# Kernel optimization log

Hardware: AMD Instinct MI355X
Metric: run time of the kernel (lower is better)

Reference implementation:

```python
import jax, jax.numpy as jnp
import numpy as np

EPS = 1e-06

def _feature_map(x):
    # elu(x) + 1, positive feature map
    return jax.nn.elu(x) + 1.0

def setup_inputs() -> dict:
    key = jax.random.key(0)
    k1, k2, k3 = jax.random.split(key, 3)
    B, L, d_k, d_v = 2, 4096, 128, 128
    Q = jax.random.normal(k1, (B, L, d_k), dtype=jnp.float32)
    K = jax.random.normal(k2, (B, L, d_k), dtype=jnp.float32)
    V = jax.random.normal(k3, (B, L, d_v), dtype=jnp.float32)
    return {"Q": Q, "K": K, "V": V}

def reference(Q, K, V):
    # Causal linear attention (ELU feature map).
    # out_l = phi(Q_l) @ sum_{j<=l} phi(K_j)^T V_j
    # Z_l   = phi(Q_l) . sum_{j<=l} phi(K_j)
    phiQ = _feature_map(Q)                       # (B, L, dk)
    phiK = _feature_map(K)                       # (B, L, dk)
    # cumulative KV state: (B, L, dk, dv) -- parallel replacement of the
    # original per-step bmm loop
    KV = jnp.cumsum(phiK[..., :, None] * V[..., None, :], axis=1)
    out = jnp.einsum('blk,blkv->blv', phiQ, KV)  # (B, L, dv)
    Kc = jnp.cumsum(phiK, axis=1)                # (B, L, dk)
    Z = jnp.einsum('blk,blk->bl', phiQ, Kc)[..., None]  # (B, L, 1)
    return out / (Z + EPS)
```

## Files before the change

### kernel.cpp

```cpp
#include <hip/hip_runtime.h>


#define EPS 1e-6f

constexpr int Bc = 2;
constexpr int L  = 4096;
constexpr int D  = 128;
constexpr int C  = 128;
constexpr int NC = L / C;
constexpr int P  = 136;

typedef short sh8 __attribute__((ext_vector_type(8)));
typedef float f4  __attribute__((ext_vector_type(4)));

__device__ __forceinline__ float phi(float x) {
    return x > 0.0f ? x + 1.0f : __expf(x);
}
__device__ __forceinline__ unsigned short f2bf(float f) {
    unsigned u = __float_as_uint(f);
    return (unsigned short)((u + 0x7FFFu + ((u >> 16) & 1u)) >> 16);
}
__device__ __forceinline__ float bf2f(unsigned short h) {
    return __uint_as_float(((unsigned)h) << 16);
}
__device__ __forceinline__ unsigned packbf(float a, float b) {
    return (unsigned)f2bf(a) | ((unsigned)f2bf(b) << 16);
}
__device__ __forceinline__ sh8 splat1() {
    sh8 s;
#pragma unroll
    for (int j = 0; j < 8; ++j) s[j] = (short)0x3F80;
    return s;
}

__global__ __launch_bounds__(512) void k1(
    const float* __restrict__ K, const float* __restrict__ V,
    unsigned short* __restrict__ SB, float* __restrict__ Ksum) {
    const int c = blockIdx.x, b = blockIdx.y, vs = blockIdx.z;
    const int tid = threadIdx.x;
    __shared__ __align__(16) unsigned short sVT[64 * P];
    __shared__ __align__(16) unsigned short sKT[128 * P];
    const size_t base = ((size_t)b * L + (size_t)c * C) * D;

    for (int k = 0; k < 4; ++k) {
        int fi = tid + 512 * k;
        int l = fi >> 4, c4 = fi & 15;
        float4 vd = *(const float4*)(V + base + (size_t)l * D + vs * 64 + c4 * 4);
        int blk = (((l >> 3) + c4) & 15) * 8 + (l & 7);
        sVT[(c4 * 4 + 0) * P + blk] = f2bf(vd.x);
        sVT[(c4 * 4 + 1) * P + blk] = f2bf(vd.y);
        sVT[(c4 * 4 + 2) * P + blk] = f2bf(vd.z);
        sVT[(c4 * 4 + 3) * P + blk] = f2bf(vd.w);
    }
    for (int k = 0; k < 8; ++k) {
        int fi = tid + 512 * k;
        int l = fi >> 5, i4 = fi & 31;
        float4 kd = *(const float4*)(K + base + (size_t)l * D + i4 * 4);
        int blk = (((l >> 3) + i4) & 15) * 8 + (l & 7);
        sKT[(i4 * 4 + 0) * P + blk] = f2bf(phi(kd.x));
        sKT[(i4 * 4 + 1) * P + blk] = f2bf(phi(kd.y));
        sKT[(i4 * 4 + 2) * P + blk] = f2bf(phi(kd.z));
        sKT[(i4 * 4 + 3) * P + blk] = f2bf(phi(kd.w));
    }
    __syncthreads();

    const int w = tid >> 6, lane = tid & 63;
    const int r = lane & 15, q = lane >> 4;
    const int rbase = (w & 3) * 16;
    const int cbase = (w >> 2) * 64;
    const bool doK = ((w & 3) == 0);
    const sh8 ones = splat1();

    f4 acc[4], kz[4];
#pragma unroll
    for (int f = 0; f < 4; ++f) { acc[f] = {0.f,0.f,0.f,0.f}; kz[f] = {0.f,0.f,0.f,0.f}; }
#pragma unroll
    for (int ks = 0; ks < 4; ++ks) {
        int kq = ks * 4 + q;
        int vr = rbase + r;
        sh8 a = *(const sh8*)(sVT + vr * P + ((kq + (vr >> 2)) & 15) * 8);
#pragma unroll
        for (int f = 0; f < 4; ++f) {
            int ir = cbase + f * 16 + r;
            sh8 bk = *(const sh8*)(sKT + ir * P + ((kq + (ir >> 2)) & 15) * 8);
            acc[f] = __builtin_amdgcn_mfma_f32_16x16x32_bf16(a, bk, acc[f], 0, 0, 0);
            if (doK) kz[f] = __builtin_amdgcn_mfma_f32_16x16x32_bf16(ones, bk, kz[f], 0, 0, 0);
        }
    }
    unsigned short* out = SB + ((size_t)(b * NC + c)) * D * D;
#pragma unroll
    for (int f = 0; f < 4; ++f) {
        int i = cbase + f * 16 + r;
#pragma unroll
        for (int e = 0; e < 4; ++e) {
            int v = vs * 64 + rbase + q * 4 + e;
            out[(size_t)v * D + i] = f2bf(acc[f][e]);
        }
    }
    if (doK && q == 0 && vs == 0) {
#pragma unroll
        for (int f = 0; f < 4; ++f)
            Ksum[((size_t)(b * NC + c)) * D + cbase + f * 16 + r] = kz[f][0];
    }
}

__global__ __launch_bounds__(256) void k_scan(unsigned short* __restrict__ SB,
                                              float* __restrict__ Ksum) {
    const int SD = D * D;
    int idx = blockIdx.x * 256 + threadIdx.x;
    if (idx < Bc * SD) {
        int b = idx / SD, e = idx % SD;
        size_t off0 = (size_t)b * NC * SD + e;
        unsigned short vals[NC];
#pragma unroll
        for (int c = 0; c < NC; ++c) vals[c] = SB[off0 + (size_t)c * SD];
        float run = 0.0f;
#pragma unroll
        for (int c = 0; c < NC; ++c) {
            SB[off0 + (size_t)c * SD] = f2bf(run);
            run += bf2f(vals[c]);
        }
    } else if (idx < Bc * SD + Bc * D) {
        int rr = idx - Bc * SD;
        int b = rr >> 7, i = rr & 127;
        size_t off0 = (size_t)b * NC * D + i;
        float vals[NC];
#pragma unroll
        for (int c = 0; c < NC; ++c) vals[c] = Ksum[off0 + (size_t)c * D];
        float run = 0.0f;
#pragma unroll
        for (int c = 0; c < NC; ++c) {
            Ksum[off0 + (size_t)c * D] = run;
            run += vals[c];
        }
    }
}

__global__ __launch_bounds__(512) void k_out(
    const float* __restrict__ Q, const float* __restrict__ K,
    const float* __restrict__ V, const unsigned short* __restrict__ SB,
    const float* __restrict__ Ksum, float* __restrict__ Out) {
    const int c = blockIdx.x, b = blockIdx.y, rs = blockIdx.z;
    const int tid = threadIdx.x;
    __shared__ __align__(16) unsigned short sQ[32 * P];
    __shared__ __align__(16) unsigned short sK[128 * P];
    __shared__ __align__(16) unsigned short sVT[128 * P];
    __shared__ __align__(16) unsigned short sAm[32 * P];
    __shared__ float sZ[32];
    const size_t base  = ((size_t)b * L + (size_t)c * C) * D;
    const size_t tbase = ((size_t)(b * NC + c)) * (size_t)D * D;
    const size_t kb    = ((size_t)(b * NC + c)) * D;

    for (int k = 0; k < 2; ++k) {
        int fi = tid + 512 * k;
        int row = fi >> 5, c4 = fi & 31;
        float4 qd = *(const float4*)(Q + base + (size_t)(rs * 32 + row) * D + c4 * 4);
        uint2 pq; pq.x = packbf(phi(qd.x), phi(qd.y)); pq.y = packbf(phi(qd.z), phi(qd.w));
        *(uint2*)(sQ + row * P + c4 * 4) = pq;
    }
    for (int k = 0; k < 8; ++k) {
        int fi = tid + 512 * k;
        int row = fi >> 5, c4 = fi & 31;
        float4 kd = *(const float4*)(K + base + (size_t)row * D + c4 * 4);
        uint2 pk; pk.x = packbf(phi(kd.x), phi(kd.y)); pk.y = packbf(phi(kd.z), phi(kd.w));
        *(uint2*)(sK + row * P + c4 * 4) = pk;
    }
    for (int k = 0; k < 8; ++k) {
        int fi = tid + 512 * k;
        int l = fi >> 5, i4 = fi & 31;
        float4 vd = *(const float4*)(V + base + (size_t)l * D + i4 * 4);
        int blk = (((l >> 3) + i4) & 15) * 8 + (l & 7);
        sVT[(i4 * 4 + 0) * P + blk] = f2bf(vd.x);
        sVT[(i4 * 4 + 1) * P + blk] = f2bf(vd.y);
        sVT[(i4 * 4 + 2) * P + blk] = f2bf(vd.z);
        sVT[(i4 * 4 + 3) * P + blk] = f2bf(vd.w);
    }
    __syncthreads();

    const int w = tid >> 6, lane = tid & 63;
    const int r = lane & 15, q = lane >> 4;
    const int rbase = (w & 1) * 16;
    const int cq = w >> 1, cbase = cq * 32;
    const bool doZ = (cq == 3);

    sh8 bzk[4];
    if (doZ) {
#pragma unroll
        for (int ks = 0; ks < 4; ++ks) {
            float4 f0 = *(const float4*)(Ksum + kb + ks * 32 + q * 8);
            float4 f1 = *(const float4*)(Ksum + kb + ks * 32 + q * 8 + 4);
            sh8 t;
            t[0] = (short)f2bf(f0.x); t[1] = (short)f2bf(f0.y);
            t[2] = (short)f2bf(f0.z); t[3] = (short)f2bf(f0.w);
            t[4] = (short)f2bf(f1.x); t[5] = (short)f2bf(f1.y);
            t[6] = (short)f2bf(f1.z); t[7] = (short)f2bf(f1.w);
            bzk[ks] = t;
        }
    }

    f4 a2[2];
#pragma unroll
    for (int f = 0; f < 2; ++f) a2[f] = {0.f,0.f,0.f,0.f};
#pragma unroll
    for (int ks = 0; ks < 4; ++ks) {
        sh8 a = *(const sh8*)(sQ + (rbase + r) * P + ks * 32 + q * 8);
#pragma unroll
        for (int f = 0; f < 2; ++f) {
            sh8 bb = *(const sh8*)(sK + (cbase + f * 16 + r) * P + ks * 32 + q * 8);
            a2[f] = __builtin_amdgcn_mfma_f32_16x16x32_bf16(a, bb, a2[f], 0, 0, 0);
        }
    }
#pragma unroll
    for (int f = 0; f < 2; ++f) {
        int j = cbase + f * 16 + r;
#pragma unroll
        for (int e = 0; e < 4; ++e) {
            int lr = rbase + q * 4 + e;
            sAm[lr * P + j] = f2bf((j <= rs * 32 + lr) ? a2[f][e] : 0.f);
        }
    }
    __syncthreads();

    {
        const uint4* sg = (const uint4*)(SB + tbase);
        for (int k = 0; k < 4; ++k) {
            int f2 = tid + 512 * k;
            *(uint4*)(sK + (f2 >> 4) * P + (f2 & 15) * 8) = sg[f2];
        }
    }

    f4 acc[2], zacc = {0.f,0.f,0.f,0.f};
#pragma unroll
    for (int f = 0; f < 2; ++f) acc[f] = {0.f,0.f,0.f,0.f};
    const sh8 ones = splat1();
#pragma unroll
    for (int ks = 0; ks < 4; ++ks) {
        int kq = ks * 4 + q;
        sh8 a = *(const sh8*)(sAm + (rbase + r) * P + ks * 32 + q * 8);
#pragma unroll
        for (int f = 0; f < 2; ++f) {
            int vr = cbase + f * 16 + r;
            sh8 bv = *(const sh8*)(sVT + vr * P + ((kq + (vr >> 2)) & 15) * 8);
            acc[f] = __builtin_amdgcn_mfma_f32_16x16x32_bf16(a, bv, acc[f], 0, 0, 0);
        }
        if (doZ) zacc = __builtin_amdgcn_mfma_f32_16x16x32_bf16(a, ones, zacc, 0, 0, 0);
    }
    __syncthreads();

#pragma unroll
    for (int ks = 0; ks < 4; ++ks) {
        sh8 a = *(const sh8*)(sQ + (rbase + r) * P + ks * 32 + q * 8);
#pragma unroll
        for (int f = 0; f < 2; ++f) {
            sh8 bs = *(const sh8*)(sK + (cbase + f * 16 + r) * P + ks * 32 + q * 8);
            acc[f] = __builtin_amdgcn_mfma_f32_16x16x32_bf16(a, bs, acc[f], 0, 0, 0);
        }
        if (doZ) zacc = __builtin_amdgcn_mfma_f32_16x16x32_bf16(a, bzk[ks], zacc, 0, 0, 0);
    }
    if (doZ && r == 0) {
#pragma unroll
        for (int e = 0; e < 4; ++e) sZ[rbase + q * 4 + e] = zacc[e] + EPS;
    }
    __syncthreads();

#pragma unroll
    for (int f = 0; f < 2; ++f) {
        int v = cbase + f * 16 + r;
#pragma unroll
        for (int e = 0; e < 4; ++e) {
            int lr = rbase + q * 4 + e;
            Out[base + (size_t)(rs * 32 + lr) * D + v] = acc[f][e] / sZ[lr];
        }
    }
}

extern "C" void kernel_launch(void* const* d_in, const int* in_sizes, int n_in,
                              void* d_out, int out_size, void* d_ws, size_t ws_size,
                              hipStream_t stream) {
    const float* Q = (const float*)d_in[0];
    const float* K = (const float*)d_in[1];
    const float* V = (const float*)d_in[2];
    float* Out = (float*)d_out;
    unsigned short* SBw = (unsigned short*)d_ws;
    float* Ksum = (float*)((char*)d_ws + (size_t)Bc * NC * D * D * 2);

    k1<<<dim3(NC, Bc, 2), 512, 0, stream>>>(K, V, SBw, Ksum);
    int total = Bc * D * D + Bc * D;
    k_scan<<<dim3((total + 255) / 256), 256, 0, stream>>>(SBw, Ksum);
    k_out<<<dim3(NC, Bc, 4), 512, 0, stream>>>(Q, K, V, SBw, Ksum, Out);
}
```

Before: 77.56 us.

## Precompute bf16 phi(K) and transposed V in k1, read directly from global in k_out

k1 now also writes bf16 phi(K) rows and the swizzled bf16 V-transpose tile to workspace. k_out drops its shared-memory staging of Q, K, V and the scan state and reads MFMA operands straight from global/L2, keeping phi(Q) fragments in registers. This removes the redundant fp32 loads and conversions of K and V that the four row-split blocks each repeated, along with several barriers. The cost is extra global writes in k1, more workspace, and uncoalesced 16-byte operand loads from L2 inside the MFMA loops.

```diff
diff --git a/kernel.cpp b/kernel.cpp
--- a/kernel.cpp
+++ b/kernel.cpp
@@ -23,9 +23,6 @@
 __device__ __forceinline__ float bf2f(unsigned short h) {
     return __uint_as_float(((unsigned)h) << 16);
 }
-__device__ __forceinline__ unsigned packbf(float a, float b) {
-    return (unsigned)f2bf(a) | ((unsigned)f2bf(b) << 16);
-}
 __device__ __forceinline__ sh8 splat1() {
     sh8 s;
 #pragma unroll
@@ -35,7 +32,8 @@
 
 __global__ __launch_bounds__(512) void k1(
     const float* __restrict__ K, const float* __restrict__ V,
-    unsigned short* __restrict__ SB, float* __restrict__ Ksum) {
+    unsigned short* __restrict__ SB, float* __restrict__ Ksum,
+    unsigned short* __restrict__ KB, unsigned short* __restrict__ VT) {
     const int c = blockIdx.x, b = blockIdx.y, vs = blockIdx.z;
     const int tid = threadIdx.x;
     __shared__ __align__(16) unsigned short sVT[64 * P];
@@ -57,12 +55,30 @@
         int l = fi >> 5, i4 = fi & 31;
         float4 kd = *(const float4*)(K + base + (size_t)l * D + i4 * 4);
         int blk = (((l >> 3) + i4) & 15) * 8 + (l & 7);
-        sKT[(i4 * 4 + 0) * P + blk] = f2bf(phi(kd.x));
-        sKT[(i4 * 4 + 1) * P + blk] = f2bf(phi(kd.y));
-        sKT[(i4 * 4 + 2) * P + blk] = f2bf(phi(kd.z));
-        sKT[(i4 * 4 + 3) * P + blk] = f2bf(phi(kd.w));
+        unsigned short h0 = f2bf(phi(kd.x)), h1 = f2bf(phi(kd.y));
+        unsigned short h2 = f2bf(phi(kd.z)), h3 = f2bf(phi(kd.w));
+        sKT[(i4 * 4 + 0) * P + blk] = h0;
+        sKT[(i4 * 4 + 1) * P + blk] = h1;
+        sKT[(i4 * 4 + 2) * P + blk] = h2;
+        sKT[(i4 * 4 + 3) * P + blk] = h3;
+        if (vs == 0) {
+            uint2 pk;
+            pk.x = (unsigned)h0 | ((unsigned)h1 << 16);
+            pk.y = (unsigned)h2 | ((unsigned)h3 << 16);
+            *(uint2*)(KB + base + (size_t)l * D + i4 * 4) = pk;
+        }
     }
     __syncthreads();
+
+    {
+        const size_t vtb = (size_t)(b * NC + c) * D * 128 + (size_t)vs * 64 * 128;
+        for (int k = 0; k < 2; ++k) {
+            int idx = tid + 512 * k;
+            int vr = idx >> 4, c8 = idx & 15;
+            *(uint4*)(VT + vtb + vr * 128 + c8 * 8) =
+                *(const uint4*)(sVT + vr * P + c8 * 8);
+        }
+    }
 
     const int w = tid >> 6, lane = tid & 63;
     const int r = lane & 15, q = lane >> 4;
@@ -137,51 +153,39 @@
 }
 
 __global__ __launch_bounds__(512) void k_out(
-    const float* __restrict__ Q, const float* __restrict__ K,
-    const float* __restrict__ V, const unsigned short* __restrict__ SB,
+    const float* __restrict__ Q, const unsigned short* __restrict__ KB,
+    const unsigned short* __restrict__ VT, const unsigned short* __restrict__ SB,
     const float* __restrict__ Ksum, float* __restrict__ Out) {
     const int c = blockIdx.x, b = blockIdx.y, rs = blockIdx.z;
     const int tid = threadIdx.x;
-    __shared__ __align__(16) unsigned short sQ[32 * P];
-    __shared__ __align__(16) unsigned short sK[128 * P];
-    __shared__ __align__(16) unsigned short sVT[128 * P];
     __shared__ __align__(16) unsigned short sAm[32 * P];
     __shared__ float sZ[32];
-    const size_t base  = ((size_t)b * L + (size_t)c * C) * D;
-    const size_t tbase = ((size_t)(b * NC + c)) * (size_t)D * D;
-    const size_t kb    = ((size_t)(b * NC + c)) * D;
-
-    for (int k = 0; k < 2; ++k) {
-        int fi = tid + 512 * k;
-        int row = fi >> 5, c4 = fi & 31;
-        float4 qd = *(const float4*)(Q + base + (size_t)(rs * 32 + row) * D + c4 * 4);
-        uint2 pq; pq.x = packbf(phi(qd.x), phi(qd.y)); pq.y = packbf(phi(qd.z), phi(qd.w));
-        *(uint2*)(sQ + row * P + c4 * 4) = pq;
-    }
-    for (int k = 0; k < 8; ++k) {
-        int fi = tid + 512 * k;
-        int row = fi >> 5, c4 = fi & 31;
-        float4 kd = *(const float4*)(K + base + (size_t)row * D + c4 * 4);
-        uint2 pk; pk.x = packbf(phi(kd.x), phi(kd.y)); pk.y = packbf(phi(kd.z), phi(kd.w));
-        *(uint2*)(sK + row * P + c4 * 4) = pk;
-    }
-    for (int k = 0; k < 8; ++k) {
-        int fi = tid + 512 * k;
-        int l = fi >> 5, i4 = fi & 31;
-        float4 vd = *(const float4*)(V + base + (size_t)l * D + i4 * 4);
-        int blk = (((l >> 3) + i4) & 15) * 8 + (l & 7);
-        sVT[(i4 * 4 + 0) * P + blk] = f2bf(vd.x);
-        sVT[(i4 * 4 + 1) * P + blk] = f2bf(vd.y);
-        sVT[(i4 * 4 + 2) * P + blk] = f2bf(vd.z);
-        sVT[(i4 * 4 + 3) * P + blk] = f2bf(vd.w);
-    }
-    __syncthreads();
+    const size_t obase = ((size_t)b * L + (size_t)c * C) * D;
+    const size_t tbase = (size_t)(b * NC + c) * (size_t)D * D;
+    const size_t vtb   = (size_t)(b * NC + c) * (size_t)D * 128;
+    const size_t kb    = (size_t)(b * NC + c) * D;
 
     const int w = tid >> 6, lane = tid & 63;
     const int r = lane & 15, q = lane >> 4;
     const int rbase = (w & 1) * 16;
     const int cq = w >> 1, cbase = cq * 32;
     const bool doZ = (cq == 3);
+
+    sh8 qf[4];
+    {
+        const float* qrow = Q + obase + (size_t)(rs * 32 + rbase + r) * D;
+#pragma unroll
+        for (int ks = 0; ks < 4; ++ks) {
+            float4 a0 = *(const float4*)(qrow + ks * 32 + q * 8);
+            float4 a1 = *(const float4*)(qrow + ks * 32 + q * 8 + 4);
+            sh8 t;
+            t[0] = (short)f2bf(phi(a0.x)); t[1] = (short)f2bf(phi(a0.y));
+            t[2] = (short)f2bf(phi(a0.z)); t[3] = (short)f2bf(phi(a0.w));
+            t[4] = (short)f2bf(phi(a1.x)); t[5] = (short)f2bf(phi(a1.y));
+            t[6] = (short)f2bf(phi(a1.z)); t[7] = (short)f2bf(phi(a1.w));
+            qf[ks] = t;
+        }
+    }
 
     sh8 bzk[4];
     if (doZ) {
@@ -203,11 +207,11 @@
     for (int f = 0; f < 2; ++f) a2[f] = {0.f,0.f,0.f,0.f};
 #pragma unroll
     for (int ks = 0; ks < 4; ++ks) {
-        sh8 a = *(const sh8*)(sQ + (rbase + r) * P + ks * 32 + q * 8);
 #pragma unroll
         for (int f = 0; f < 2; ++f) {
-            sh8 bb = *(const sh8*)(sK + (cbase + f * 16 + r) * P + ks * 32 + q * 8);
-            a2[f] = __builtin_amdgcn_mfma_f32_16x16x32_bf16(a, bb, a2[f], 0, 0, 0);
+            int j = cbase + f * 16 + r;
+            sh8 bb = *(const sh8*)(KB + obase + (size_t)j * D + ks * 32 + q * 8);
+            a2[f] = __builtin_amdgcn_mfma_f32_16x16x32_bf16(qf[ks], bb, a2[f], 0, 0, 0);
         }
     }
 #pragma unroll
@@ -221,14 +225,6 @@
     }
     __syncthreads();
 
-    {
-        const uint4* sg = (const uint4*)(SB + tbase);
-        for (int k = 0; k < 4; ++k) {
-            int f2 = tid + 512 * k;
-            *(uint4*)(sK + (f2 >> 4) * P + (f2 & 15) * 8) = sg[f2];
-        }
-    }
-
     f4 acc[2], zacc = {0.f,0.f,0.f,0.f};
 #pragma unroll
     for (int f = 0; f < 2; ++f) acc[f] = {0.f,0.f,0.f,0.f};
@@ -240,22 +236,22 @@
 #pragma unroll
         for (int f = 0; f < 2; ++f) {
             int vr = cbase + f * 16 + r;
-            sh8 bv = *(const sh8*)(sVT + vr * P + ((kq + (vr >> 2)) & 15) * 8);
+            sh8 bv = *(const sh8*)(VT + vtb + (size_t)vr * 128 +
+                                   ((kq + (vr >> 2)) & 15) * 8);
             acc[f] = __builtin_amdgcn_mfma_f32_16x16x32_bf16(a, bv, acc[f], 0, 0, 0);
         }
         if (doZ) zacc = __builtin_amdgcn_mfma_f32_16x16x32_bf16(a, ones, zacc, 0, 0, 0);
     }
-    __syncthreads();
-
-#pragma unroll
-    for (int ks = 0; ks < 4; ++ks) {
-        sh8 a = *(const sh8*)(sQ + (rbase + r) * P + ks * 32 + q * 8);
+
+#pragma unroll
+    for (int ks = 0; ks < 4; ++ks) {
 #pragma unroll
         for (int f = 0; f < 2; ++f) {
-            sh8 bs = *(const sh8*)(sK + (cbase + f * 16 + r) * P + ks * 32 + q * 8);
-            acc[f] = __builtin_amdgcn_mfma_f32_16x16x32_bf16(a, bs, acc[f], 0, 0, 0);
-        }
-        if (doZ) zacc = __builtin_amdgcn_mfma_f32_16x16x32_bf16(a, bzk[ks], zacc, 0, 0, 0);
+            int v = cbase + f * 16 + r;
+            sh8 bs = *(const sh8*)(SB + tbase + (size_t)v * D + ks * 32 + q * 8);
+            acc[f] = __builtin_amdgcn_mfma_f32_16x16x32_bf16(qf[ks], bs, acc[f], 0, 0, 0);
+        }
+        if (doZ) zacc = __builtin_amdgcn_mfma_f32_16x16x32_bf16(qf[ks], bzk[ks], zacc, 0, 0, 0);
     }
     if (doZ && r == 0) {
 #pragma unroll
@@ -269,7 +265,7 @@
 #pragma unroll
         for (int e = 0; e < 4; ++e) {
             int lr = rbase + q * 4 + e;
-            Out[base + (size_t)(rs * 32 + lr) * D + v] = acc[f][e] / sZ[lr];
+            Out[obase + (size_t)(rs * 32 + lr) * D + v] = acc[f][e] / sZ[lr];
         }
     }
 }
@@ -281,11 +277,14 @@
     const float* K = (const float*)d_in[1];
     const float* V = (const float*)d_in[2];
     float* Out = (float*)d_out;
+    const size_t SB_BYTES = (size_t)Bc * NC * D * D * 2;
     unsigned short* SBw = (unsigned short*)d_ws;
-    float* Ksum = (float*)((char*)d_ws + (size_t)Bc * NC * D * D * 2);
-
-    k1<<<dim3(NC, Bc, 2), 512, 0, stream>>>(K, V, SBw, Ksum);
+    unsigned short* KBw = (unsigned short*)((char*)d_ws + SB_BYTES);
+    unsigned short* VTw = (unsigned short*)((char*)d_ws + 2 * SB_BYTES);
+    float* Ksum = (float*)((char*)d_ws + 3 * SB_BYTES);
+
+    k1<<<dim3(NC, Bc, 2), 512, 0, stream>>>(K, V, SBw, Ksum, KBw, VTw);
     int total = Bc * D * D + Bc * D;
     k_scan<<<dim3((total + 255) / 256), 256, 0, stream>>>(SBw, Ksum);
-    k_out<<<dim3(NC, Bc, 4), 512, 0, stream>>>(Q, K, V, SBw, Ksum, Out);
-}
+    k_out<<<dim3(NC, Bc, 4), 512, 0, stream>>>(Q, KBw, VTw, SBw, Ksum, Out);
+}
```

New measurement: 83.68 us. 1.08x slower.
